# Kernel tuning notes

Hardware: AMD Instinct MI355X
Metric: run time of the kernel (lower is better)

## Reference

```python
import jax, jax.numpy as jnp
import numpy as np

N, L, D = 1024, 128, 512
H = D // 2  # LSTM hidden per direction


def _lstm_dir(x, w_ih, w_hh, b_ih, b_hh, reverse=False):
    # x: [B, T, Din] -> [B, T, H]; PyTorch gate order i, f, g, o
    B = x.shape[0]
    Hh = w_hh.shape[1]
    xs = jnp.swapaxes(x, 0, 1)  # [T, B, Din]
    if reverse:
        xs = xs[::-1]
    pre = jnp.einsum('tbi,gi->tbg', xs, w_ih) + b_ih  # precompute input contribution

    def step(carry, p):
        h, c = carry
        g = p + h @ w_hh.T + b_hh
        i, f, cc, o = jnp.split(g, 4, axis=-1)
        c = jax.nn.sigmoid(f) * c + jax.nn.sigmoid(i) * jnp.tanh(cc)
        h = jax.nn.sigmoid(o) * jnp.tanh(c)
        return (h, c), h

    zeros = jnp.zeros((B, Hh), x.dtype)
    _, hs = jax.lax.scan(step, (zeros, zeros), pre)
    if reverse:
        hs = hs[::-1]
    return jnp.swapaxes(hs, 0, 1)


def _bilstm(x, params):
    # params: [(w_ih, w_hh, b_ih, b_hh)] for l0_fwd, l0_bwd, l1_fwd, l1_bwd
    for lf, lb in ((params[0], params[1]), (params[2], params[3])):
        f = _lstm_dir(x, *lf)
        b = _lstm_dir(x, *lb, reverse=True)
        x = jnp.concatenate([f, b], axis=-1)
    return x


def _forward(episodes, query, current_state, ages, Wq, bq, Wk, bk, lstm_params, k):
    # retrieve_relevant_episodes: batched version of the per-episode loop
    query_proj = query @ Wq.T + bq              # [D]
    emb = episodes.mean(axis=1)                 # [N, D] per-episode mean embedding
    key_proj = emb @ Wk.T + bk                  # [N, D]
    scores = key_proj @ query_proj              # [N] (matmul(q, kp.T).mean() == dot for 1D)
    _, idx = jax.lax.top_k(scores, k)           # descending, == argsort[-k:][::-1]
    sel = jnp.take(episodes, idx, axis=0)       # [k, L, D]
    # temporal_attention
    w = 1.0 / (1.0 + jnp.take(ages, idx) * 0.01)  # temporal recency weight
    x = sel * w[:, None, None]
    lstm_out = _bilstm(x, lstm_params)          # [k, L, D]
    att = jnp.einsum('d,kld->kl', current_state, lstm_out)  # [k, L] (== [k,1,L])
    attw = jax.nn.softmax(att, axis=-1)
    context = jnp.einsum('kl,kld->kd', attw, lstm_out)[:, None, :]  # [k, 1, D]
    return context


def setup_inputs() -> dict:
    key = jax.random.key(0)
    ks = jax.random.split(key, 32)
    s = 1.0 / np.sqrt(D)
    sh = 1.0 / np.sqrt(H)
    inp = {
        'episodes': jax.random.normal(ks[0], (N, L, D), jnp.float32),
        'query': jax.random.normal(ks[1], (D,), jnp.float32),
        'current_state': jax.random.normal(ks[2], (D,), jnp.float32),
        'ages': jax.random.uniform(ks[3], (N,), jnp.float32) * 100.0,
        'Wq': jax.random.normal(ks[4], (D, D), jnp.float32) * s,
        'bq': jnp.zeros((D,), jnp.float32),
        'Wk': jax.random.normal(ks[5], (D, D), jnp.float32) * s,
        'bk': jnp.zeros((D,), jnp.float32),
    }
    i = 6
    for name in ['l0', 'l0r', 'l1', 'l1r']:
        inp['w_ih_' + name] = jax.random.normal(ks[i], (4 * H, D), jnp.float32) * sh; i += 1
        inp['w_hh_' + name] = jax.random.normal(ks[i], (4 * H, H), jnp.float32) * sh; i += 1
        inp['b_ih_' + name] = jnp.zeros((4 * H,), jnp.float32)
        inp['b_hh_' + name] = jnp.zeros((4 * H,), jnp.float32)
    inp['k'] = 5
    return inp


def reference(episodes, query, current_state, ages, Wq, bq, Wk, bk,
              w_ih_l0, w_hh_l0, b_ih_l0, b_hh_l0,
              w_ih_l0r, w_hh_l0r, b_ih_l0r, b_hh_l0r,
              w_ih_l1, w_hh_l1, b_ih_l1, b_hh_l1,
              w_ih_l1r, w_hh_l1r, b_ih_l1r, b_hh_l1r, k):
    lstm_params = [
        (w_ih_l0, w_hh_l0, b_ih_l0, b_hh_l0),
        (w_ih_l0r, w_hh_l0r, b_ih_l0r, b_hh_l0r),
        (w_ih_l1, w_hh_l1, b_ih_l1, b_hh_l1),
        (w_ih_l1r, w_hh_l1r, b_ih_l1r, b_hh_l1r),
    ]
    return _forward(episodes, query, current_state, ages, Wq, bq, Wk, bk, lstm_params, k)
```

## Files before the change

kernel.cpp:

```cpp
#include <hip/hip_runtime.h>
#include <hip/hip_bf16.h>
#include <math.h>

typedef unsigned short u16;
typedef unsigned int   u32;
typedef unsigned long long u64;

#define DEV static __device__ __forceinline__

static constexpr int LL = 128, DD = 512, HH = 256, KK = 5, NN = 1024;

static constexpr size_t OFF_QP   = 0;
static constexpr size_t OFF_U    = 4096;
static constexpr size_t OFF_CC   = 8192;
static constexpr size_t OFF_SC   = 12288;
static constexpr size_t OFF_WSC  = 16384;
static constexpr size_t OFF_IDX  = 16640;
static constexpr size_t OFF_HG   = 20480;
static constexpr size_t OFF_FLG0 = 61440;
static constexpr size_t OFF_FLG1 = 65536;
static constexpr size_t OFF_CNT  = 69632;
static constexpr size_t OFF_PRE  = 73728;
static constexpr size_t OFF_OUT0 = OFF_PRE  + (size_t)2*LL*5*1024*4;
static constexpr size_t OFF_OUT1 = OFF_OUT0 + (size_t)5*LL*DD*4;

DEV float sigf(float x){ return 1.0f/(1.0f + expf(-x)); }

DEV float ald(const float* p) {
  return __hip_atomic_load(p, __ATOMIC_RELAXED, __HIP_MEMORY_SCOPE_AGENT);
}
DEV void ast(float* p, float v) {
  __hip_atomic_store(p, v, __ATOMIC_RELAXED, __HIP_MEMORY_SCOPE_AGENT);
}
template<int SLP>
DEV void wait_ge(int* p, int v) {
  while (__hip_atomic_load(p, __ATOMIC_RELAXED, __HIP_MEMORY_SCOPE_AGENT) < v)
    __builtin_amdgcn_s_sleep(SLP);
}

__global__ __launch_bounds__(256) void k_front(
    const float* __restrict__ Wq, const float* __restrict__ qu,
    const float* __restrict__ bq, const float* __restrict__ Wk,
    const float* __restrict__ bk, const float* __restrict__ ep,
    const float* __restrict__ ages,
    float* __restrict__ qp, float* __restrict__ u, float* __restrict__ cconst,
    float* __restrict__ scores, int* __restrict__ idx5, float* __restrict__ wsc,
    int* __restrict__ cnt) {
  __shared__ float qs[512];
  __shared__ float red2[16][17];
  __shared__ float r2[256];
  __shared__ float redS[256];
  __shared__ float s0[NN];
  __shared__ float sv[256];
  __shared__ int   si[256];
  __shared__ int   chosen[KK];
  int bid = blockIdx.x, tid = threadIdx.x;

  if (bid < 64) {
    qs[tid] = qu[tid]; qs[tid+256] = qu[tid+256];
    __syncthreads();
    int row = bid*8 + (tid >> 5), lane = tid & 31;
    const float* wr = Wq + (size_t)row*512 + lane*16;
    float acc = 0.f;
    #pragma unroll
    for (int j = 0; j < 16; j += 4) {
      float4 w = *(const float4*)(wr + j);
      acc += w.x*qs[lane*16+j] + w.y*qs[lane*16+j+1] + w.z*qs[lane*16+j+2] + w.w*qs[lane*16+j+3];
    }
    #pragma unroll
    for (int off = 16; off > 0; off >>= 1) acc += __shfl_down(acc, off, 32);
    if (lane == 0) ast(&qp[row], acc + bq[row]);
    __syncthreads();
    if (tid == 0) __hip_atomic_fetch_add(&cnt[0], 1, __ATOMIC_RELAXED, __HIP_MEMORY_SCOPE_AGENT);
    __syncthreads();
  }

  if (bid >= 64 && bid < 96) {
    if (tid == 0) wait_ge<2>(&cnt[0], 64);
    __syncthreads();
    qs[tid] = ald(&qp[tid]); qs[tid+256] = ald(&qp[tid+256]);
    __syncthreads();
    int kb = bid - 64;
    int cl = tid & 15, jc = tid >> 4;
    int col = kb*16 + cl;
    float acc = 0.f;
    for (int j = jc*32; j < jc*32 + 32; ++j) acc += Wk[(size_t)j*512 + col] * qs[j];
    red2[cl][jc] = acc;
    __syncthreads();
    if (tid < 16) {
      float a = 0.f;
      #pragma unroll
      for (int m = 0; m < 16; ++m) a += red2[tid][m];
      ast(&u[kb*16 + tid], a);
    }
    if (kb == 0) {
      float b2 = bk[tid]*qs[tid] + bk[tid+256]*qs[tid+256];
      r2[tid] = b2;
      __syncthreads();
      for (int off = 128; off > 0; off >>= 1) { if (tid < off) r2[tid] += r2[tid+off]; __syncthreads(); }
      if (tid == 0) ast(&cconst[0], r2[0]);
    }
    __syncthreads();
    if (tid == 0) __hip_atomic_fetch_add(&cnt[1], 1, __ATOMIC_RELAXED, __HIP_MEMORY_SCOPE_AGENT);
    __syncthreads();
  }

  {
    if (tid == 0) wait_ge<32>(&cnt[1], 32);
    __syncthreads();
    int d0 = (tid * 4) & 511;
    float u0 = ald(&u[d0+0]), u1 = ald(&u[d0+1]), u2 = ald(&u[d0+2]), u3 = ald(&u[d0+3]);
    float ccv = ald(cconst);
    const float* base = ep + (size_t)bid * (LL*DD);
    float acc = 0.f;
    for (int c = tid; c < (LL*DD)/4; c += 256) {
      float4 v = *(const float4*)(base + (size_t)c*4);
      acc += v.x*u0 + v.y*u1 + v.z*u2 + v.w*u3;
    }
    redS[tid] = acc;
    __syncthreads();
    for (int off = 128; off > 0; off >>= 1) { if (tid < off) redS[tid] += redS[tid+off]; __syncthreads(); }
    if (tid == 0) ast(&scores[bid], redS[0] * (1.0f/LL) + ccv);
    __syncthreads();
    if (tid == 0) __hip_atomic_fetch_add(&cnt[2], 1, __ATOMIC_RELAXED, __HIP_MEMORY_SCOPE_AGENT);
  }

  if (bid == 0) {
    if (tid == 0) wait_ge<8>(&cnt[2], NN);
    __syncthreads();
    #pragma unroll
    for (int k = 0; k < 4; ++k) s0[tid + k*256] = ald(&scores[tid + k*256]);
    __syncthreads();
    for (int r = 0; r < KK; ++r) {
      float bv = -3.4e38f; int bi = 0x7fffffff;
      #pragma unroll
      for (int k = 0; k < 4; ++k) {
        int i = tid + k*256;
        float v = s0[i];
        bool excl = false;
        for (int m = 0; m < r; ++m) excl = excl || (chosen[m] == i);
        if (!excl && (v > bv || (v == bv && i < bi))) { bv = v; bi = i; }
      }
      sv[tid] = bv; si[tid] = bi;
      __syncthreads();
      for (int off = 128; off > 0; off >>= 1) {
        if (tid < off) {
          float b = sv[tid+off]; int ib = si[tid+off];
          if (b > sv[tid] || (b == sv[tid] && ib < si[tid])) { sv[tid] = b; si[tid] = ib; }
        }
        __syncthreads();
      }
      if (tid == 0) {
        int w = si[0];
        chosen[r] = w;
        idx5[r] = w;
        wsc[r] = 1.0f / (1.0f + ages[w] * 0.01f);
      }
      __syncthreads();
    }
  }
}

__global__ __launch_bounds__(256) void k_pre(
    const float* __restrict__ ep, const float* __restrict__ x1,
    const int* __restrict__ idx5, const float* __restrict__ wsc,
    const float* __restrict__ wihF, const float* __restrict__ wihB,
    const float* __restrict__ bihF, const float* __restrict__ bhhF,
    const float* __restrict__ bihB, const float* __restrict__ bhhB,
    float* __restrict__ pre) {
  int t = blockIdx.x, dir = blockIdx.y;
  int tid = threadIdx.x;
  __shared__ __align__(16) float xs[5*512];
  if (ep) {
    for (int f = tid; f < 5*512; f += 256) {
      int b = f >> 9, i = f & 511;
      xs[f] = ep[((size_t)idx5[b]*LL + t)*DD + i] * wsc[b];
    }
  } else {
    for (int f = tid; f < 5*512; f += 256) {
      int b = f >> 9, i = f & 511;
      xs[f] = x1[((size_t)b*LL + t)*DD + i];
    }
  }
  const float* wih = dir ? wihB : wihF;
  const float* bih = dir ? bihB : bihF;
  const float* bhh = dir ? bhhB : bhhF;
  __syncthreads();

  const float4* w4 = (const float4*)wih;
  const float4* x4 = (const float4*)xs;
  float acc[4][5];
  #pragma unroll
  for (int g = 0; g < 4; ++g)
    #pragma unroll
    for (int b = 0; b < 5; ++b) acc[g][b] = 0.f;

  #pragma unroll 4
  for (int kq = 0; kq < 128; ++kq) {
    float4 xv[5];
    #pragma unroll
    for (int b = 0; b < 5; ++b) xv[b] = x4[b*128 + kq];
    #pragma unroll
    for (int g = 0; g < 4; ++g) {
      float4 w = w4[(size_t)(tid + g*256)*128 + kq];
      #pragma unroll
      for (int b = 0; b < 5; ++b) {
        acc[g][b] += w.x*xv[b].x + w.y*xv[b].y + w.z*xv[b].z + w.w*xv[b].w;
      }
    }
  }

  size_t pbase = (((size_t)dir*LL + t)*5)*1024;
  #pragma unroll
  for (int g = 0; g < 4; ++g) {
    int row = tid + g*256;
    float bias = bih[row] + bhh[row];
    #pragma unroll
    for (int b = 0; b < 5; ++b)
      pre[pbase + (size_t)b*1024 + row] = acc[g][b] + bias;
  }
}

__global__ __launch_bounds__(1024) void k_lstm(
    const float* __restrict__ whhF, const float* __restrict__ whhB,
    const float* __restrict__ pre, float* __restrict__ out,
    float* __restrict__ hg, int* __restrict__ flg) {
  int wg  = blockIdx.x;
  int dir = wg >> 3;
  int q   = wg & 7;
  int tid = threadIdx.x;
  int rp  = tid & 63;
  int jq  = tid >> 6;
  int jb  = jq * 16;
  const float* whh = dir ? whhB : whhF;

  __shared__ __align__(16) float h_lds[5*256];
  __shared__ __align__(16) float part[5*16*130];
  __shared__ float c_s[5*32];
  __shared__ float pre_lds[5*128];

  int r0 = 2*rp, r1 = 2*rp + 1;
  int gr0 = (r0 >> 5)*256 + q*32 + (r0 & 31);
  int gr1 = (r1 >> 5)*256 + q*32 + (r1 & 31);
  float w0[16], w1[16];
  #pragma unroll
  for (int m4 = 0; m4 < 4; ++m4) {
    float4 a = *(const float4*)(whh + (size_t)gr0*256 + jb + m4*4);
    w0[m4*4+0]=a.x; w0[m4*4+1]=a.y; w0[m4*4+2]=a.z; w0[m4*4+3]=a.w;
    float4 c = *(const float4*)(whh + (size_t)gr1*256 + jb + m4*4);
    w1[m4*4+0]=c.x; w1[m4*4+1]=c.y; w1[m4*4+2]=c.z; w1[m4*4+3]=c.w;
  }
  for (int f = tid; f < 1280; f += 1024) h_lds[f] = 0.f;
  if (tid < 160) c_s[tid] = 0.f;
  float* hg_dir = hg + (size_t)dir * 2 * 1280;
  int*  flg_dir = flg + dir * 64;
  __syncthreads();

  for (int s = 0; s < LL; ++s) {
    int t = dir ? (LL-1-s) : s;
    if (tid < 640) {
      int b = tid >> 7, r = tid & 127;
      int grow = (r >> 5)*256 + q*32 + (r & 31);
      pre_lds[tid] = pre[(((size_t)dir*LL + t)*5 + b)*1024 + grow];
    }
    if (s > 0) {
      const float* hrd = hg_dir + (size_t)(s & 1) * 1280;
      if (tid < 8) {
        while (__hip_atomic_load(&flg_dir[tid], __ATOMIC_RELAXED,
                                 __HIP_MEMORY_SCOPE_AGENT) < s) {}
      }
      __syncthreads();
      for (int f = tid; f < 1120; f += 1024) {
        int b = f / 224, w2 = f % 224;
        int c7 = w2 >> 5, u = w2 & 31;
        int pch = c7 + (c7 >= q);
        int idx = b*256 + pch*32 + u;
        h_lds[idx] = __hip_atomic_load(&hrd[idx], __ATOMIC_RELAXED,
                                       __HIP_MEMORY_SCOPE_AGENT);
      }
    }
    __syncthreads();
    {
      float acc0[5], acc1[5];
      #pragma unroll
      for (int b = 0; b < 5; ++b) {
        const float4* h4 = (const float4*)&h_lds[b*256 + jb];
        float a0 = 0.f, a1 = 0.f;
        #pragma unroll
        for (int m4 = 0; m4 < 4; ++m4) {
          float4 hv = h4[m4];
          a0 += w0[m4*4+0]*hv.x + w0[m4*4+1]*hv.y + w0[m4*4+2]*hv.z + w0[m4*4+3]*hv.w;
          a1 += w1[m4*4+0]*hv.x + w1[m4*4+1]*hv.y + w1[m4*4+2]*hv.z + w1[m4*4+3]*hv.w;
        }
        acc0[b] = a0; acc1[b] = a1;
      }
      #pragma unroll
      for (int b = 0; b < 5; ++b) {
        *(float2*)&part[(b*16 + jq)*130 + 2*rp] = make_float2(acc0[b], acc1[b]);
      }
    }
    __syncthreads();
    if (tid < 160) {
      int b = tid >> 5, u = tid & 31;
      float g[4];
      #pragma unroll
      for (int gate = 0; gate < 4; ++gate) {
        int r = gate*32 + u;
        float sum = pre_lds[b*128 + r];
        #pragma unroll
        for (int m = 0; m < 16; ++m) sum += part[(b*16 + m)*130 + r];
        g[gate] = sum;
      }
      float ig = sigf(g[0]), fg = sigf(g[1]), cc = tanhf(g[2]), og = sigf(g[3]);
      float cn = fg * c_s[b*32 + u] + ig * cc;
      c_s[b*32 + u] = cn;
      float hv = og * tanhf(cn);
      out[((size_t)b*LL + t)*DD + dir*HH + q*32 + u] = hv;
      h_lds[b*256 + q*32 + u] = hv;
      float* hwr = hg_dir + (size_t)((s + 1) & 1) * 1280;
      __hip_atomic_store(&hwr[b*256 + q*32 + u], hv,
                         __ATOMIC_RELAXED, __HIP_MEMORY_SCOPE_AGENT);
    }
    __syncthreads();
    if (tid == 0)
      __hip_atomic_store(&flg_dir[q], s + 1, __ATOMIC_RELAXED,
                         __HIP_MEMORY_SCOPE_AGENT);
  }
}

__global__ void k_attn(const float* __restrict__ out1, const float* __restrict__ csb,
                       float* __restrict__ outp) {
  int b = blockIdx.x, tid = threadIdx.x;
  __shared__ float cs[512];
  __shared__ float att[128];
  __shared__ float red[256];
  __shared__ float smax, ssum;
  cs[tid] = csb[tid]; cs[tid+256] = csb[tid+256];
  __syncthreads();
  {
    int t = tid & 127, half = tid >> 7;
    const float* row = out1 + ((size_t)b*LL + t)*DD + half*256;
    const float* c2 = cs + half*256;
    float a = 0.f;
    for (int d = 0; d < 256; ++d) a += row[d] * c2[d];
    red[tid] = a;
  }
  __syncthreads();
  if (tid < 128) att[tid] = red[tid] + red[tid+128];
  __syncthreads();
  if (tid < 64) red[tid] = fmaxf(att[tid], att[tid+64]);
  __syncthreads();
  if (tid == 0) { float m = red[0]; for (int o = 1; o < 64; ++o) m = fmaxf(m, red[o]); smax = m; }
  __syncthreads();
  if (tid < 128) att[tid] = expf(att[tid] - smax);
  __syncthreads();
  if (tid < 64) red[tid] = att[tid] + att[tid+64];
  __syncthreads();
  if (tid == 0) { float s = 0.f; for (int o = 0; o < 64; ++o) s += red[o]; ssum = s; }
  __syncthreads();
  float inv = 1.0f / ssum;
  for (int d = tid; d < DD; d += 256) {
    float acc = 0.f;
    for (int t2 = 0; t2 < LL; ++t2) acc += att[t2] * out1[((size_t)b*LL + t2)*DD + d];
    outp[b*DD + d] = acc * inv;
  }
}

extern "C" void kernel_launch(void* const* d_in, const int* in_sizes, int n_in,
                              void* d_out, int out_size, void* d_ws, size_t ws_size,
                              hipStream_t stream) {
  (void)in_sizes; (void)n_in; (void)out_size; (void)ws_size;
  const float* ep   = (const float*)d_in[0];
  const float* qu   = (const float*)d_in[1];
  const float* cst  = (const float*)d_in[2];
  const float* ages = (const float*)d_in[3];
  const float* Wq   = (const float*)d_in[4];
  const float* bq   = (const float*)d_in[5];
  const float* Wk   = (const float*)d_in[6];
  const float* bk   = (const float*)d_in[7];
  const float *wih[4], *whh[4], *bih[4], *bhh[4];
  for (int l = 0; l < 4; ++l) {
    wih[l] = (const float*)d_in[8 + l*4 + 0];
    whh[l] = (const float*)d_in[8 + l*4 + 1];
    bih[l] = (const float*)d_in[8 + l*4 + 2];
    bhh[l] = (const float*)d_in[8 + l*4 + 3];
  }
  char* ws = (char*)d_ws;
  float* qp   = (float*)(ws + OFF_QP);
  float* uvec = (float*)(ws + OFF_U);
  float* cc   = (float*)(ws + OFF_CC);
  float* sc   = (float*)(ws + OFF_SC);
  float* wsc  = (float*)(ws + OFF_WSC);
  int*   idx5 = (int*)  (ws + OFF_IDX);
  float* hg0  = (float*)(ws + OFF_HG);
  float* hg1  = (float*)(ws + OFF_HG + 20480);
  int*   flg0 = (int*)  (ws + OFF_FLG0);
  int*   flg1 = (int*)  (ws + OFF_FLG1);
  int*   cnt  = (int*)  (ws + OFF_CNT);
  float* pre  = (float*)(ws + OFF_PRE);
  float* out0 = (float*)(ws + OFF_OUT0);
  float* out1 = (float*)(ws + OFF_OUT1);

  (void)hipMemsetAsync(ws + OFF_FLG0, 0, 12288, stream);

  k_front<<<NN, 256, 0, stream>>>(Wq, qu, bq, Wk, bk, ep, ages,
                                  qp, uvec, cc, sc, idx5, wsc, cnt);

  k_pre <<<dim3(LL,2), 256, 0, stream>>>(ep, nullptr, idx5, wsc,
        wih[0], wih[1], bih[0], bhh[0], bih[1], bhh[1], pre);
  k_lstm<<<16, 1024, 0, stream>>>(whh[0], whh[1], pre, out0, hg0, flg0);

  k_pre <<<dim3(LL,2), 256, 0, stream>>>(nullptr, out0, idx5, wsc,
        wih[2], wih[3], bih[2], bhh[2], bih[3], bhh[3], pre);
  k_lstm<<<16, 1024, 0, stream>>>(whh[2], whh[3], pre, out1, hg1, flg1);

  k_attn<<<KK, 256, 0, stream>>>(out1, cst, (float*)d_out);
}
```

Before: 1.443 ms.

## Fuse layer-0 input projection into front kernel and attention into final LSTM

The layer-0 input-projection work (formerly a separate k_pre launch) now runs inside k_front: blocks 0-255 spin-wait on a counter set after top-k selection, then compute the pre-activations. The attention/softmax tail is folded into the second k_lstm launch, where the first five workgroups poll all direction flags, then compute attention over the LSTM output using atomic loads. This removes two kernel launches and their gaps. In exchange it adds intra-kernel spin waits that depend on the waiting blocks and the block that signals them being co-resident. It also adds extra shared memory to k_front and k_lstm, which could lower occupancy.

```diff
diff --git a/kernel.cpp b/kernel.cpp
--- a/kernel.cpp
+++ b/kernel.cpp
@@ -32,6 +32,12 @@
 DEV void ast(float* p, float v) {
   __hip_atomic_store(p, v, __ATOMIC_RELAXED, __HIP_MEMORY_SCOPE_AGENT);
 }
+DEV int aldi(const int* p) {
+  return __hip_atomic_load(p, __ATOMIC_RELAXED, __HIP_MEMORY_SCOPE_AGENT);
+}
+DEV void asti(int* p, int v) {
+  __hip_atomic_store(p, v, __ATOMIC_RELAXED, __HIP_MEMORY_SCOPE_AGENT);
+}
 template<int SLP>
 DEV void wait_ge(int* p, int v) {
   while (__hip_atomic_load(p, __ATOMIC_RELAXED, __HIP_MEMORY_SCOPE_AGENT) < v)
@@ -45,7 +51,11 @@
     const float* __restrict__ ages,
     float* __restrict__ qp, float* __restrict__ u, float* __restrict__ cconst,
     float* __restrict__ scores, int* __restrict__ idx5, float* __restrict__ wsc,
-    int* __restrict__ cnt) {
+    int* __restrict__ cnt,
+    const float* __restrict__ wihF, const float* __restrict__ wihB,
+    const float* __restrict__ bihF, const float* __restrict__ bhhF,
+    const float* __restrict__ bihB, const float* __restrict__ bhhB,
+    float* __restrict__ pre) {
   __shared__ float qs[512];
   __shared__ float red2[16][17];
   __shared__ float r2[256];
@@ -54,6 +64,7 @@
   __shared__ float sv[256];
   __shared__ int   si[256];
   __shared__ int   chosen[KK];
+  __shared__ __align__(16) float xs[5*512];
   int bid = blockIdx.x, tid = threadIdx.x;
 
   if (bid < 64) {
@@ -153,10 +164,57 @@
       if (tid == 0) {
         int w = si[0];
         chosen[r] = w;
-        idx5[r] = w;
-        wsc[r] = 1.0f / (1.0f + ages[w] * 0.01f);
+        asti(&idx5[r], w);
+        ast(&wsc[r], 1.0f / (1.0f + ages[w] * 0.01f));
       }
       __syncthreads();
+    }
+    if (tid == 0) __hip_atomic_fetch_add(&cnt[3], 1, __ATOMIC_RELAXED, __HIP_MEMORY_SCOPE_AGENT);
+  }
+
+  if (bid < 256) {
+    if (tid == 0) wait_ge<4>(&cnt[3], 1);
+    __syncthreads();
+    int t = bid & 127, dir = bid >> 7;
+    int id5[5]; float wv5[5];
+    #pragma unroll
+    for (int b = 0; b < 5; ++b) { id5[b] = aldi(&idx5[b]); wv5[b] = ald(&wsc[b]); }
+    for (int f = tid; f < 5*512; f += 256) {
+      int b = f >> 9, i = f & 511;
+      xs[f] = ep[((size_t)id5[b]*LL + t)*DD + i] * wv5[b];
+    }
+    const float* wih = dir ? wihB : wihF;
+    const float* bih = dir ? bihB : bihF;
+    const float* bhh = dir ? bhhB : bhhF;
+    __syncthreads();
+    const float4* w4 = (const float4*)wih;
+    const float4* x4 = (const float4*)xs;
+    float acc[4][5];
+    #pragma unroll
+    for (int g = 0; g < 4; ++g)
+      #pragma unroll
+      for (int b = 0; b < 5; ++b) acc[g][b] = 0.f;
+    #pragma unroll 4
+    for (int kq = 0; kq < 128; ++kq) {
+      float4 xv[5];
+      #pragma unroll
+      for (int b = 0; b < 5; ++b) xv[b] = x4[b*128 + kq];
+      #pragma unroll
+      for (int g = 0; g < 4; ++g) {
+        float4 w = w4[(size_t)(tid + g*256)*128 + kq];
+        #pragma unroll
+        for (int b = 0; b < 5; ++b)
+          acc[g][b] += w.x*xv[b].x + w.y*xv[b].y + w.z*xv[b].z + w.w*xv[b].w;
+      }
+    }
+    size_t pbase = (((size_t)dir*LL + t)*5)*1024;
+    #pragma unroll
+    for (int g = 0; g < 4; ++g) {
+      int row = tid + g*256;
+      float bias = bih[row] + bhh[row];
+      #pragma unroll
+      for (int b = 0; b < 5; ++b)
+        pre[pbase + (size_t)b*1024 + row] = acc[g][b] + bias;
     }
   }
 }
@@ -224,7 +282,8 @@
 __global__ __launch_bounds__(1024) void k_lstm(
     const float* __restrict__ whhF, const float* __restrict__ whhB,
     const float* __restrict__ pre, float* __restrict__ out,
-    float* __restrict__ hg, int* __restrict__ flg) {
+    float* __restrict__ hg, int* __restrict__ flg,
+    const float* __restrict__ csb, float* __restrict__ outp, int doattn) {
   int wg  = blockIdx.x;
   int dir = wg >> 3;
   int q   = wg & 7;
@@ -238,6 +297,11 @@
   __shared__ __align__(16) float part[5*16*130];
   __shared__ float c_s[5*32];
   __shared__ float pre_lds[5*128];
+  __shared__ float cs_l[512];
+  __shared__ float red9[128*9];
+  __shared__ float att[128];
+  __shared__ float redA[64];
+  __shared__ float smax, ssum;
 
   int r0 = 2*rp, r1 = 2*rp + 1;
   int gr0 = (r0 >> 5)*256 + q*32 + (r0 & 31);
@@ -315,7 +379,7 @@
       float cn = fg * c_s[b*32 + u] + ig * cc;
       c_s[b*32 + u] = cn;
       float hv = og * tanhf(cn);
-      out[((size_t)b*LL + t)*DD + dir*HH + q*32 + u] = hv;
+      ast(&out[((size_t)b*LL + t)*DD + dir*HH + q*32 + u], hv);
       h_lds[b*256 + q*32 + u] = hv;
       float* hwr = hg_dir + (size_t)((s + 1) & 1) * 1280;
       __hip_atomic_store(&hwr[b*256 + q*32 + u], hv,
@@ -326,43 +390,49 @@
       __hip_atomic_store(&flg_dir[q], s + 1, __ATOMIC_RELAXED,
                          __HIP_MEMORY_SCOPE_AGENT);
   }
-}
-
-__global__ void k_attn(const float* __restrict__ out1, const float* __restrict__ csb,
-                       float* __restrict__ outp) {
-  int b = blockIdx.x, tid = threadIdx.x;
-  __shared__ float cs[512];
-  __shared__ float att[128];
-  __shared__ float red[256];
-  __shared__ float smax, ssum;
-  cs[tid] = csb[tid]; cs[tid+256] = csb[tid+256];
-  __syncthreads();
-  {
-    int t = tid & 127, half = tid >> 7;
-    const float* row = out1 + ((size_t)b*LL + t)*DD + half*256;
-    const float* c2 = cs + half*256;
-    float a = 0.f;
-    for (int d = 0; d < 256; ++d) a += row[d] * c2[d];
-    red[tid] = a;
-  }
-  __syncthreads();
-  if (tid < 128) att[tid] = red[tid] + red[tid+128];
-  __syncthreads();
-  if (tid < 64) red[tid] = fmaxf(att[tid], att[tid+64]);
-  __syncthreads();
-  if (tid == 0) { float m = red[0]; for (int o = 1; o < 64; ++o) m = fmaxf(m, red[o]); smax = m; }
-  __syncthreads();
-  if (tid < 128) att[tid] = expf(att[tid] - smax);
-  __syncthreads();
-  if (tid < 64) red[tid] = att[tid] + att[tid+64];
-  __syncthreads();
-  if (tid == 0) { float s = 0.f; for (int o = 0; o < 64; ++o) s += red[o]; ssum = s; }
-  __syncthreads();
-  float inv = 1.0f / ssum;
-  for (int d = tid; d < DD; d += 256) {
-    float acc = 0.f;
-    for (int t2 = 0; t2 < LL; ++t2) acc += att[t2] * out1[((size_t)b*LL + t2)*DD + d];
-    outp[b*DD + d] = acc * inv;
+
+  if (doattn && wg < 5) {
+    if (tid < 16) {
+      int* fp = flg + (tid >> 3) * 64 + (tid & 7);
+      while (__hip_atomic_load(fp, __ATOMIC_RELAXED,
+                               __HIP_MEMORY_SCOPE_AGENT) < LL) {}
+    }
+    if (tid < 512) cs_l[tid] = csb[tid];
+    __syncthreads();
+    int b = wg;
+    const float* ob = out + (size_t)b*LL*DD;
+    {
+      int t = tid & 127, seg = tid >> 7;
+      const float* rowp = ob + (size_t)t*DD + seg*64;
+      const float* c2 = cs_l + seg*64;
+      float a = 0.f;
+      for (int d = 0; d < 64; ++d) a += ald(&rowp[d]) * c2[d];
+      red9[t*9 + seg] = a;
+    }
+    __syncthreads();
+    if (tid < 128) {
+      float s2 = 0.f;
+      #pragma unroll
+      for (int m = 0; m < 8; ++m) s2 += red9[tid*9 + m];
+      att[tid] = s2;
+    }
+    __syncthreads();
+    if (tid < 64) redA[tid] = fmaxf(att[tid], att[tid+64]);
+    __syncthreads();
+    if (tid == 0) { float m = redA[0]; for (int o = 1; o < 64; ++o) m = fmaxf(m, redA[o]); smax = m; }
+    __syncthreads();
+    if (tid < 128) att[tid] = expf(att[tid] - smax);
+    __syncthreads();
+    if (tid < 64) redA[tid] = att[tid] + att[tid+64];
+    __syncthreads();
+    if (tid == 0) { float s2 = 0.f; for (int o = 0; o < 64; ++o) s2 += redA[o]; ssum = s2; }
+    __syncthreads();
+    if (tid < 512) {
+      float inv = 1.0f / ssum;
+      float a = 0.f;
+      for (int t2 = 0; t2 < 128; ++t2) a += att[t2] * ald(&ob[(size_t)t2*DD + tid]);
+      outp[b*DD + tid] = a * inv;
+    }
   }
 }
 
@@ -404,15 +474,16 @@
   (void)hipMemsetAsync(ws + OFF_FLG0, 0, 12288, stream);
 
   k_front<<<NN, 256, 0, stream>>>(Wq, qu, bq, Wk, bk, ep, ages,
-                                  qp, uvec, cc, sc, idx5, wsc, cnt);
-
-  k_pre <<<dim3(LL,2), 256, 0, stream>>>(ep, nullptr, idx5, wsc,
-        wih[0], wih[1], bih[0], bhh[0], bih[1], bhh[1], pre);
-  k_lstm<<<16, 1024, 0, stream>>>(whh[0], whh[1], pre, out0, hg0, flg0);
+                                  qp, uvec, cc, sc, idx5, wsc, cnt,
+                                  wih[0], wih[1], bih[0], bhh[0], bih[1], bhh[1],
+                                  pre);
+
+  k_lstm<<<16, 1024, 0, stream>>>(whh[0], whh[1], pre, out0, hg0, flg0,
+                                  nullptr, nullptr, 0);
 
   k_pre <<<dim3(LL,2), 256, 0, stream>>>(nullptr, out0, idx5, wsc,
         wih[2], wih[3], bih[2], bhh[2], bih[3], bhh[3], pre);
-  k_lstm<<<16, 1024, 0, stream>>>(whh[2], whh[3], pre, out1, hg1, flg1);
-
-  k_attn<<<KK, 256, 0, stream>>>(out1, cst, (float*)d_out);
-}
+
+  k_lstm<<<16, 1024, 0, stream>>>(whh[2], whh[3], pre, out1, hg1, flg1,
+                                  cst, (float*)d_out, 1);
+}
```

Measured after the change: 1.495 ms. 3.6% more time.
